# Kernel optimization log

Measured on AMD Instinct MI355X. Metric: run time of the kernel, lower is better.

The kernel has to match this reference:

```python
import jax, jax.numpy as jnp
import numpy as np

NUM_PRIMARY_CAPS = 8
PRIMARY_DIM = 8
NUM_CLASSES = 10
OUT_DIM = 16
CHANNELS = 32
NUM_ROUTING = 3
IN_UNITS1 = CHANNELS * 20 * 20  # 12800


def squash(s):
    # squash as written in the source: |s| / (1 + |s|^2) * s
    n = jnp.linalg.norm(s, axis=-1, keepdims=True)
    return n / (1.0 + n * n) * s


def routing(u_hat, num_routing):
    # u_hat: [B, num_caps, in_units, dim_caps]
    b = jnp.zeros(u_hat.shape[:3] + (1,), dtype=u_hat.dtype)
    v = None
    for it in range(num_routing):
        c = jax.nn.softmax(b, axis=1)                       # over num_caps
        s = jnp.sum(c * u_hat, axis=2, keepdims=True)        # [B,J,1,M]
        v = squash(s)
        if it < num_routing - 1:
            b = b + jnp.sum(u_hat * v, axis=-1, keepdims=True)
    return v[:, :, 0, :]                                     # [B, num_caps, dim_caps]


def setup_inputs() -> dict:
    key = jax.random.key(0)
    k1, k2, k3, k4, k5 = jax.random.split(key, 5)
    x = jax.random.normal(k1, (64, 1, 28, 28), dtype=jnp.float32)
    conv_w = jax.random.normal(k2, (CHANNELS, 1, 9, 9), dtype=jnp.float32) * 0.05
    conv_b = jax.random.normal(k3, (CHANNELS,), dtype=jnp.float32) * 0.05
    # W: [num_capsules, in_units, dim_capsules, in_channels]
    W1 = jax.random.normal(k4, (NUM_PRIMARY_CAPS, IN_UNITS1, PRIMARY_DIM, CHANNELS), dtype=jnp.float32) * 0.05
    W2 = jax.random.normal(k5, (NUM_CLASSES, NUM_PRIMARY_CAPS, OUT_DIM, PRIMARY_DIM), dtype=jnp.float32) * 0.05
    return {"x": x, "conv_w": conv_w, "conv_b": conv_b, "W1": W1, "W2": W2}


def reference(x, conv_w, conv_b, W1, W2):
    B = x.shape[0]
    # conv1 + relu: [B,1,28,28] -> [B,C,20,20]
    h = jax.lax.conv_general_dilated(
        x, conv_w, window_strides=(1, 1), padding='VALID',
        dimension_numbers=('NCHW', 'OIHW', 'NCHW'))
    h = jax.nn.relu(h + conv_b[None, :, None, None])
    # primary capsules: flatten features to in_units; the source einsum
    # 'ijkl,ijkm->ijkm' reduces W over its in_channels axis and broadcasts x,
    # so u_hat[b,j,k,m] = sum_c W1[j,k,m,c] * x[b,k]
    xf = h.reshape(B, IN_UNITS1)
    u1 = jnp.einsum('jkmc,bk->bjkm', W1, xf)   # [B, 8, 12800, primary_dim]
    v1 = routing(u1, 1)                         # [B, 8, primary_dim]
    # digit capsules: per-unit feature vectors, standard capsule transform
    u2 = jnp.einsum('jkmc,bkc->bjkm', W2, v1)   # [B, 10, 8, out_dim]
    v2 = routing(u2, NUM_ROUTING)               # [B, 10, out_dim]
    return v2
```

## Files before the change

kernel.cpp:

```cpp
#include <hip/hip_runtime.h>

typedef float f4 __attribute__((ext_vector_type(4)));

__device__ __forceinline__ float readlane_f(float v, int l) {
    return __int_as_float(__builtin_amdgcn_readlane(__float_as_int(v), l));
}

__global__ __launch_bounds__(512) void fused_kernel(
    const float* __restrict__ X, const float* __restrict__ CW, const float* __restrict__ CB,
    const float* __restrict__ W1, float* __restrict__ S1P)
{
    int i = blockIdx.x;
    int c = i >> 3, p0 = (i & 7) * 50;
    int t = threadIdx.x;
    int wave = t >> 6, lane = t & 63;

    __shared__ float xs[32][309];
    __shared__ float xt[50][64];

    int py0 = p0 / 20;

    float bias = CB[c];
    const float* wcg = CW + c * 81;
    float w[81];
    #pragma unroll
    for (int q = 0; q < 81; ++q) w[q] = wcg[q];

    for (int h = 0; h < 2; ++h) {
        {
            int b = t >> 4, q = t & 15;
            const f4* src = reinterpret_cast<const f4*>(X + (size_t)(b + 32 * h) * 784 + py0 * 28);
            #pragma unroll
            for (int it2 = 0; it2 < 5; ++it2) {
                int idx4 = q + 16 * it2;
                if (idx4 < 77) {
                    f4 v = src[idx4];
                    float* d = &xs[b][idx4 * 4];
                    d[0] = v.x; d[1] = v.y; d[2] = v.z; d[3] = v.w;
                }
            }
        }
        __syncthreads();
        {
            int psub = t >> 5, b = t & 31;
            for (int pl = psub; pl < 50; pl += 16) {
                int p = p0 + pl;
                int py = p / 20, px = p - py * 20;
                const float* xrow = &xs[b][(py - py0) * 28 + px];
                float acc = bias;
                #pragma unroll
                for (int dy = 0; dy < 9; ++dy)
                    #pragma unroll
                    for (int dx = 0; dx < 9; ++dx)
                        acc = fmaf(xrow[dy * 28 + dx], w[dy * 9 + dx], acc);
                xt[pl][b + 32 * h] = acc > 0.f ? acc : 0.f;
            }
        }
        __syncthreads();
    }

    int k0 = c * 400 + p0;
    const f4* Wp = reinterpret_cast<const f4*>(W1) + (size_t)wave * 819200
                   + (size_t)k0 * 64 + lane;
    float acc[8] = {0.f,0.f,0.f,0.f,0.f,0.f,0.f,0.f};
    #pragma unroll 10
    for (int kk = 0; kk < 50; ++kk) {
        f4 wv = __builtin_nontemporal_load(Wp); Wp += 64;
        float xv = xt[kk][lane];
        float s = (wv.x + wv.y) + (wv.z + wv.w);
        s += __shfl_xor(s, 1);
        s += __shfl_xor(s, 2);
        s += __shfl_xor(s, 4);
        #pragma unroll
        for (int m = 0; m < 8; ++m)
            acc[m] = fmaf(xv, readlane_f(s, m * 8), acc[m]);
    }

    float* dst = S1P + ((((size_t)i * 8 + wave) * 64 + lane) * 8);
    f4 lo = {acc[0], acc[1], acc[2], acc[3]};
    f4 hi = {acc[4], acc[5], acc[6], acc[7]};
    reinterpret_cast<f4*>(dst)[0] = lo;
    reinterpret_cast<f4*>(dst)[1] = hi;
}

__global__ __launch_bounds__(256) void routing_kernel(
    const float* __restrict__ W2, const float* __restrict__ S1P,
    float* __restrict__ OUT)
{
    int b = blockIdx.x;
    int t = threadIdx.x;
    __shared__ float part[64][4];
    __shared__ float v1[64];
    __shared__ float u2[10][8][16];
    __shared__ float blog[10][8];
    __shared__ float cw[10][8];
    __shared__ float sv[10][16];
    __shared__ float vv[10][16];
    __shared__ float fac[16];

    {
        int jm = t >> 2, r = t & 3;
        int j = jm >> 3, m = jm & 7;
        size_t base = (size_t)j * 512 + (size_t)b * 8 + m;
        float ssum = 0.f;
        #pragma unroll 16
        for (int ii = r; ii < 256; ii += 4)
            ssum += S1P[base + (size_t)ii * 4096];
        part[jm][r] = ssum;
    }
    __syncthreads();
    if (t < 64) v1[t] = (part[t][0] + part[t][1] + part[t][2] + part[t][3]) * 0.125f;
    if (t >= 64 && t < 144) { int q = t - 64; blog[q >> 3][q & 7] = 0.f; }
    __syncthreads();
    if (t < 8) {
        float n2 = 0.f;
        #pragma unroll
        for (int m = 0; m < 8; ++m) { float x = v1[t * 8 + m]; n2 = fmaf(x, x, n2); }
        float n = sqrtf(n2);
        fac[t] = n / (1.f + n2);
    }
    __syncthreads();
    if (t < 64) v1[t] *= fac[t >> 3];
    __syncthreads();

    for (int idx = t; idx < 1280; idx += 256) {
        int j = idx >> 7;
        int r = idx & 127;
        int k = r >> 4, m = r & 15;
        const float* wp = W2 + idx * 8;
        float a = 0.f;
        #pragma unroll
        for (int cc = 0; cc < 8; ++cc) a = fmaf(wp[cc], v1[k * 8 + cc], a);
        u2[j][k][m] = a;
    }
    __syncthreads();

    for (int it = 0; it < 3; ++it) {
        if (t < 8) {
            float mx = -1e30f;
            #pragma unroll
            for (int j = 0; j < 10; ++j) mx = fmaxf(mx, blog[j][t]);
            float e[10], se = 0.f;
            #pragma unroll
            for (int j = 0; j < 10; ++j) { e[j] = expf(blog[j][t] - mx); se += e[j]; }
            float inv = 1.f / se;
            #pragma unroll
            for (int j = 0; j < 10; ++j) cw[j][t] = e[j] * inv;
        }
        __syncthreads();
        if (t < 160) {
            int j = t >> 4, m = t & 15;
            float a = 0.f;
            #pragma unroll
            for (int k = 0; k < 8; ++k) a = fmaf(cw[j][k], u2[j][k][m], a);
            sv[j][m] = a;
        }
        __syncthreads();
        if (t < 10) {
            float n2 = 0.f;
            #pragma unroll
            for (int m = 0; m < 16; ++m) { float x = sv[t][m]; n2 = fmaf(x, x, n2); }
            float n = sqrtf(n2);
            fac[t] = n / (1.f + n2);
        }
        __syncthreads();
        if (t < 160) { int j = t >> 4, m = t & 15; vv[j][m] = sv[j][m] * fac[j]; }
        __syncthreads();
        if (it < 2) {
            if (t < 80) {
                int j = t >> 3, k = t & 7;
                float d = 0.f;
                #pragma unroll
                for (int m = 0; m < 16; ++m) d = fmaf(u2[j][k][m], vv[j][m], d);
                blog[j][k] += d;
            }
            __syncthreads();
        }
    }
    if (t < 160) OUT[b * 160 + t] = vv[t >> 4][t & 15];
}

extern "C" void kernel_launch(void* const* d_in, const int* in_sizes, int n_in,
                              void* d_out, int out_size, void* d_ws, size_t ws_size,
                              hipStream_t stream) {
    const float* X  = (const float*)d_in[0];
    const float* CW = (const float*)d_in[1];
    const float* CB = (const float*)d_in[2];
    const float* W1 = (const float*)d_in[3];
    const float* W2 = (const float*)d_in[4];
    float* S1P = (float*)d_ws;
    float* OUT = (float*)d_out;

    fused_kernel<<<256, 512, 0, stream>>>(X, CW, CB, W1, S1P);
    routing_kernel<<<64, 256, 0, stream>>>(W2, S1P, OUT);
}
```

Baseline: 168.6 us.

## Prefetch W1 before conv, single-pass conv over 64 batches, coalesce S1P layout

Issues the first ten W1 tile loads into registers before the convolution so the streaming weight reads overlap the conv compute. The conv now stages all 64 batch rows into a doubled shared buffer in one pass, using a lighter waitcnt+barrier instead of two __syncthreads rounds. The partial-sum layout in S1P is reordered so the routing kernel reads contiguous float4 vectors with wider parallel reduction. This raises LDS use (about 79KB per block) and register pressure from the ten prefetched vectors, which could lower occupancy.

```diff
diff --git a/kernel.cpp b/kernel.cpp
--- a/kernel.cpp
+++ b/kernel.cpp
@@ -4,6 +4,10 @@
 
 __device__ __forceinline__ float readlane_f(float v, int l) {
     return __int_as_float(__builtin_amdgcn_readlane(__float_as_int(v), l));
+}
+
+__device__ __forceinline__ void barrier_lds() {
+    asm volatile("s_waitcnt lgkmcnt(0)\n\ts_barrier" ::: "memory");
 }
 
 __global__ __launch_bounds__(512) void fused_kernel(
@@ -15,10 +19,18 @@
     int t = threadIdx.x;
     int wave = t >> 6, lane = t & 63;
 
-    __shared__ float xs[32][309];
+    __shared__ float xs[64][309];
     __shared__ float xt[50][64];
 
     int py0 = p0 / 20;
+
+    int k0 = c * 400 + p0;
+    const f4* Wp = reinterpret_cast<const f4*>(W1) + (size_t)wave * 819200
+                   + (size_t)k0 * 64 + lane;
+    f4 pre[10];
+    #pragma unroll
+    for (int q = 0; q < 10; ++q)
+        pre[q] = __builtin_nontemporal_load(Wp + (size_t)q * 64);
 
     float bias = CB[c];
     const float* wcg = CW + c * 81;
@@ -26,45 +38,54 @@
     #pragma unroll
     for (int q = 0; q < 81; ++q) w[q] = wcg[q];
 
-    for (int h = 0; h < 2; ++h) {
-        {
-            int b = t >> 4, q = t & 15;
-            const f4* src = reinterpret_cast<const f4*>(X + (size_t)(b + 32 * h) * 784 + py0 * 28);
-            #pragma unroll
-            for (int it2 = 0; it2 < 5; ++it2) {
-                int idx4 = q + 16 * it2;
-                if (idx4 < 77) {
-                    f4 v = src[idx4];
-                    float* d = &xs[b][idx4 * 4];
-                    d[0] = v.x; d[1] = v.y; d[2] = v.z; d[3] = v.w;
-                }
+    {
+        int b = t >> 3, q = t & 7;
+        const f4* src = reinterpret_cast<const f4*>(X + (size_t)b * 784 + py0 * 28);
+        #pragma unroll
+        for (int s = 0; s < 10; ++s) {
+            int idx4 = q + 8 * s;
+            if (idx4 < 77) {
+                f4 v = src[idx4];
+                float* d = &xs[b][idx4 * 4];
+                d[0] = v.x; d[1] = v.y; d[2] = v.z; d[3] = v.w;
             }
         }
-        __syncthreads();
-        {
-            int psub = t >> 5, b = t & 31;
-            for (int pl = psub; pl < 50; pl += 16) {
-                int p = p0 + pl;
-                int py = p / 20, px = p - py * 20;
-                const float* xrow = &xs[b][(py - py0) * 28 + px];
-                float acc = bias;
+    }
+    barrier_lds();
+
+    {
+        int psub = wave, b = lane;
+        for (int pl = psub; pl < 50; pl += 8) {
+            int p = p0 + pl;
+            int py = p / 20, px = p - py * 20;
+            const float* xrow = &xs[b][(py - py0) * 28 + px];
+            float acc = bias;
+            #pragma unroll
+            for (int dy = 0; dy < 9; ++dy)
                 #pragma unroll
-                for (int dy = 0; dy < 9; ++dy)
-                    #pragma unroll
-                    for (int dx = 0; dx < 9; ++dx)
-                        acc = fmaf(xrow[dy * 28 + dx], w[dy * 9 + dx], acc);
-                xt[pl][b + 32 * h] = acc > 0.f ? acc : 0.f;
-            }
-        }
-        __syncthreads();
-    }
-
-    int k0 = c * 400 + p0;
-    const f4* Wp = reinterpret_cast<const f4*>(W1) + (size_t)wave * 819200
-                   + (size_t)k0 * 64 + lane;
+                for (int dx = 0; dx < 9; ++dx)
+                    acc = fmaf(xrow[dy * 28 + dx], w[dy * 9 + dx], acc);
+            xt[pl][b] = acc > 0.f ? acc : 0.f;
+        }
+    }
+    barrier_lds();
+
     float acc[8] = {0.f,0.f,0.f,0.f,0.f,0.f,0.f,0.f};
+    #pragma unroll
+    for (int kk = 0; kk < 10; ++kk) {
+        f4 wv = pre[kk];
+        float xv = xt[kk][lane];
+        float s = (wv.x + wv.y) + (wv.z + wv.w);
+        s += __shfl_xor(s, 1);
+        s += __shfl_xor(s, 2);
+        s += __shfl_xor(s, 4);
+        #pragma unroll
+        for (int m = 0; m < 8; ++m)
+            acc[m] = fmaf(xv, readlane_f(s, m * 8), acc[m]);
+    }
+    Wp += (size_t)10 * 64;
     #pragma unroll 10
-    for (int kk = 0; kk < 50; ++kk) {
+    for (int kk = 10; kk < 50; ++kk) {
         f4 wv = __builtin_nontemporal_load(Wp); Wp += 64;
         float xv = xt[kk][lane];
         float s = (wv.x + wv.y) + (wv.z + wv.w);
@@ -76,7 +97,7 @@
             acc[m] = fmaf(xv, readlane_f(s, m * 8), acc[m]);
     }
 
-    float* dst = S1P + ((((size_t)i * 8 + wave) * 64 + lane) * 8);
+    float* dst = S1P + (((size_t)i * 64 + lane) * 8 + wave) * 8;
     f4 lo = {acc[0], acc[1], acc[2], acc[3]};
     f4 hi = {acc[4], acc[5], acc[6], acc[7]};
     reinterpret_cast<f4*>(dst)[0] = lo;
@@ -89,7 +110,7 @@
 {
     int b = blockIdx.x;
     int t = threadIdx.x;
-    __shared__ float part[64][4];
+    __shared__ float part[16][64];
     __shared__ float v1[64];
     __shared__ float u2[10][8][16];
     __shared__ float blog[10][8];
@@ -99,17 +120,24 @@
     __shared__ float fac[16];
 
     {
-        int jm = t >> 2, r = t & 3;
-        int j = jm >> 3, m = jm & 7;
-        size_t base = (size_t)j * 512 + (size_t)b * 8 + m;
-        float ssum = 0.f;
-        #pragma unroll 16
-        for (int ii = r; ii < 256; ii += 4)
-            ssum += S1P[base + (size_t)ii * 4096];
-        part[jm][r] = ssum;
-    }
-    __syncthreads();
-    if (t < 64) v1[t] = (part[t][0] + part[t][1] + part[t][2] + part[t][3]) * 0.125f;
+        int q = t & 15, r = t >> 4;
+        const f4* base = reinterpret_cast<const f4*>(S1P) + ((size_t)r * 64 + b) * 16 + q;
+        f4 a = {0.f, 0.f, 0.f, 0.f};
+        #pragma unroll
+        for (int s = 0; s < 16; ++s)
+            a += base[(size_t)s * 16384];
+        part[r][q * 4 + 0] = a.x;
+        part[r][q * 4 + 1] = a.y;
+        part[r][q * 4 + 2] = a.z;
+        part[r][q * 4 + 3] = a.w;
+    }
+    __syncthreads();
+    if (t < 64) {
+        float v = 0.f;
+        #pragma unroll
+        for (int r = 0; r < 16; ++r) v += part[r][t];
+        v1[t] = v * 0.125f;
+    }
     if (t >= 64 && t < 144) { int q = t - 64; blog[q >> 3][q & 7] = 0.f; }
     __syncthreads();
     if (t < 8) {
```

Result: no change. 165.5 us (-1.9%).
